# Kernel optimization log

Measured on AMD Instinct MI355X. Metric: run time of the kernel, lower is better.

Reference implementation:

```python
import jax, jax.numpy as jnp
import numpy as np
from jax import lax

H = 1024
W = 1024
WIN = 32
STR = 16
NH = (H - WIN) // STR + 1  # 63
N = NH * NH                # 3969 patches
DN3 = ('NCDHW', 'OIDHW', 'NCDHW')
DN2 = ('NCHW', 'OIHW', 'NCHW')


def setup_inputs() -> dict:
    key = jax.random.key(0)
    ks = jax.random.split(key, 13)
    r = lambda k, s, sc=0.05: jax.random.normal(k, s, dtype=jnp.float32) * sc
    return {
        'x1': jax.random.normal(ks[0], (1, 1, 1, H, W), jnp.float32),
        'x2': jax.random.normal(ks[1], (1, 1, 1, H, W), jnp.float32),
        'conv1_w': r(ks[2], (24, 1, 2, 8, 8)),      # Conv3d(1,24,(2,8,8)) [O,I,D,H,W]
        'conv1_b': r(ks[3], (24,)),
        'conv2_w': r(ks[4], (60, 24, 5, 5)),         # Conv2d(24,60,5)
        'conv2_b': r(ks[5], (60,)),
        'deconv2_w': r(ks[6], (60, 24, 5, 5)),       # ConvTranspose2d(60,24,5) [I,O,kH,kW]
        'deconv2_b': r(ks[7], (24,)),
        'deconv1_w': r(ks[8], (24, 1, 2, 8, 8)),     # ConvTranspose3d(24,1,(2,8,8)) [I,O,D,H,W]
        'deconv1_b': r(ks[9], (1,)),
        'lin_w': r(ks[10], (N, 2), 0.5),             # per-patch Linear(2,1) weights
        'lin_b': r(ks[11], (N,), 0.5),               # per-patch Linear(2,1) bias
        'linear1_w': r(ks[12], (1, 1), 0.5),         # Linear(1,1,bias=False)
    }


def _conv(x, w, b, dn):
    nd = w.ndim - 2
    y = lax.conv_general_dilated(x, w, (1,) * nd, 'VALID', dimension_numbers=dn)
    return y + b.reshape((1, -1) + (1,) * nd)


def _convT(x, w, b, dn):
    # stride-1, pad-0 transposed conv == full-pad conv with flipped, IO-swapped kernel
    nd = w.ndim - 2
    wf = jnp.flip(w, axis=tuple(range(2, w.ndim))).swapaxes(0, 1)  # [O,I,*k]
    pad = [(k - 1, k - 1) for k in w.shape[2:]]
    y = lax.conv_general_dilated(x, wf, (1,) * nd, pad, dimension_numbers=dn)
    return y + b.reshape((1, -1) + (1,) * nd)


def reference(x1, x2, conv1_w, conv1_b, conv2_w, conv2_b, deconv2_w, deconv2_b,
              deconv1_w, deconv1_b, lin_w, lin_b, linear1_w):
    x = jnp.concatenate([x1, x2], axis=2)[0, 0]  # [2,H,W]
    idx = (jnp.arange(NH) * STR)[:, None] + jnp.arange(WIN)[None, :]  # [NH,32]
    # unfold dims 3,4 with window 32 / stride 16 -> [2,NH,NW,32,32]
    patches = x[:, idx[:, None, :, None], idx[None, :, None, :]]
    outX = patches.reshape(2, N, WIN, WIN).transpose(1, 0, 2, 3)[:, None]  # [N,1,2,32,32]
    h = jax.nn.elu(_conv(outX, conv1_w, conv1_b, DN3))        # [N,24,1,25,25]
    h = jax.nn.relu(_conv(h[:, :, 0], conv2_w, conv2_b, DN2))  # [N,60,21,21]
    h = jax.nn.elu(_convT(h, deconv2_w, deconv2_b, DN2))       # [N,24,25,25]
    h = _convT(h[:, :, None], deconv1_w, deconv1_b, DN3)       # [N,1,2,32,32]
    # per-patch Linear(2,1) over depth channels, batched over all patches
    p = jnp.einsum('nchw,nc->nhw', h[:, 0], lin_w) + lin_b[:, None, None]  # [N,32,32]
    p = p.reshape(NH, NH, WIN, WIN)
    # col2im: overlap-add fold, block 32, stride 16 -> [H,W]
    recon = jnp.zeros((H, W), jnp.float32).at[idx[:, None, :, None], idx[None, :, None, :]].add(p)
    outX2 = recon * linear1_w[0, 0]  # Linear(1,1,bias=False) per pixel
    return x2 - outX2.reshape(x2.shape)
```

## Files before the change

### kernel.cpp

```cpp
#include <hip/hip_runtime.h>
#include <hip/hip_bf16.h>

static constexpr int H_ = 1024;
static constexpr int W_ = 1024;
static constexpr int STR_ = 16;
static constexpr int NH_ = 63;
static constexpr int NPATCH_ = NH_ * NH_;

typedef short bf16x8 __attribute__((ext_vector_type(8)));
typedef short short4v __attribute__((ext_vector_type(4)));
typedef float f32x4 __attribute__((ext_vector_type(4)));

static constexpr size_t FRAG_BYTES = 212992;
static constexpr size_t H1_SLAB    = 30768;
static constexpr size_t H2_SLAB    = 53248;
static constexpr size_t H1_BYTES   = (size_t)NPATCH_ * H1_SLAB;
static constexpr size_t H2_BYTES   = (size_t)NPATCH_ * H2_SLAB;
static constexpr size_t WS_NEED    = FRAG_BYTES + H1_BYTES + H2_BYTES;

__device__ __forceinline__ unsigned short f2bf(float x) {
    __hip_bfloat16 b = __float2bfloat16(x);
    return __builtin_bit_cast(unsigned short, b);
}

__device__ __forceinline__ f32x4 mfma_bf16(bf16x8 a, bf16x8 b, f32x4 c) {
    return __builtin_amdgcn_mfma_f32_16x16x32_bf16(a, b, c, 0, 0, 0);
}

__device__ __forceinline__ float elu_neg(float x) { return __expf(x) - 1.f; }

__global__ __launch_bounds__(256) void k_conv1(
    const float* __restrict__ x1, const float* __restrict__ x2,
    const float* __restrict__ c1b, const unsigned short* __restrict__ w1frag,
    unsigned short* __restrict__ h1)
{
    __shared__ alignas(16) char sbuf[10240];
    const int n = blockIdx.x, t = (int)threadIdx.x;
    const int pi = n / NH_, pj = n % NH_;
    const int Y0 = pi * STR_, X0 = pj * STR_;
    const int wv = t >> 6, lane = t & 63;
    const int ln15 = lane & 15, quad = lane >> 4;
    unsigned short* h1n = h1 + (size_t)n * (H1_SLAB / 2);

    bf16x8 w1b[8];
    #pragma unroll
    for (int g = 0; g < 8; ++g)
        w1b[g] = *(const bf16x8*)(w1frag + (g * 64 + lane) * 8);
    const f32x4 c1bq0 = *(const f32x4*)(c1b + quad * 4);
    f32x4 c1bq1 = (f32x4){0.f, 0.f, 0.f, 0.f};
    if (quad < 2) c1bq1 = *(const f32x4*)(c1b + 16 + quad * 4);

    if (t < 6) ((unsigned long long*)(h1n + 625 * 24))[t] = 0ull;

    for (int k = t; k < 2048; k += 256) {
        int d = k >> 10, r = k & 1023, y = r >> 5, x = r & 31;
        unsigned short bb = f2bf((d ? x2 : x1)[(Y0 + y) * W_ + (X0 + x)]);
        int row = (d * 32 + y) * 40;
        ((unsigned short*)(sbuf))[row + x] = bb;
        if (x > 0) ((unsigned short*)(sbuf + 5120))[row + x - 1] = bb;
    }
    __syncthreads();

    for (int tl = wv; tl < 40; tl += 4) {
        const int rawm = tl * 16 + ln15;
        int m = rawm > 624 ? 624 : rawm;
        int u = m / 25, v = m - u * 25;
        const char* cps = sbuf + ((v & 1) ? 5120 : 0);
        const int vb2 = (v & ~1) * 2;
        f32x4 acc0 = (f32x4){0.f, 0.f, 0.f, 0.f};
        f32x4 acc1 = (f32x4){0.f, 0.f, 0.f, 0.f};
        #pragma unroll
        for (int kc = 0; kc < 4; ++kc) {
            const int idx8 = kc * 4 + quad;
            const int dd = idx8 >> 3, pp = idx8 & 7;
            const unsigned int* ap = (const unsigned int*)(cps + (dd * 32 + u + pp) * 80 + vb2);
            union { unsigned int u4[4]; bf16x8 v8; } af;
            af.u4[0] = ap[0]; af.u4[1] = ap[1]; af.u4[2] = ap[2]; af.u4[3] = ap[3];
            acc0 = mfma_bf16(w1b[kc * 2 + 0], af.v8, acc0);
            acc1 = mfma_bf16(w1b[kc * 2 + 1], af.v8, acc1);
        }
        if (rawm < 625) {
            unsigned short* rowp = h1n + rawm * 24;
            short4v p0;
            #pragma unroll
            for (int r = 0; r < 4; ++r) {
                float hv = acc0[r] + c1bq0[r];
                hv = hv > 0.f ? hv : elu_neg(hv);
                p0[r] = (short)f2bf(hv);
            }
            *(short4v*)(rowp + quad * 4) = p0;
            if (quad < 2) {
                short4v p1;
                #pragma unroll
                for (int r = 0; r < 4; ++r) {
                    float hw = acc1[r] + c1bq1[r];
                    hw = hw > 0.f ? hw : elu_neg(hw);
                    p1[r] = (short)f2bf(hw);
                }
                *(short4v*)(rowp + 16 + quad * 4) = p1;
            }
        }
    }
}

__global__ __launch_bounds__(256) void k_conv2(
    const float* __restrict__ c2b, const unsigned short* __restrict__ w2frag,
    const unsigned short* __restrict__ h1, unsigned short* __restrict__ h2)
{
    __shared__ alignas(16) char sbuf[30048];
    const int n = blockIdx.x, t = (int)threadIdx.x;
    const int wv = t >> 6, lane = t & 63;
    const int ln15 = lane & 15, quad = lane >> 4;
    {
        const f32x4* src = (const f32x4*)(h1 + (size_t)n * (H1_SLAB / 2));
        f32x4* dst = (f32x4*)sbuf;
        for (int i = t; i < 1878; i += 256) dst[i] = src[i];
    }
    __syncthreads();

    const unsigned short* wb = w2frag + lane * 8;
    unsigned short* h2n = h2 + (size_t)n * (H2_SLAB / 2);

    for (int mt = wv; mt < 28; mt += 4) {
        int mm = mt * 16 + ln15; if (mm > 440) mm = 440;
        int y = mm / 21, x = mm - y * 21;
        const int abase = (y * 25 + x) * 48;
        f32x4 acc[4];
        #pragma unroll
        for (int nt = 0; nt < 4; ++nt) acc[nt] = (f32x4){0.f, 0.f, 0.f, 0.f};
        #pragma unroll
        for (int p = 0; p < 5; ++p) {
            #pragma unroll
            for (int q = 0; q < 5; ++q) {
                const int tap  = p * 5 + q;
                const int toff = (p * 25 + q) * 48;
                bf16x8 bfr[4];
                #pragma unroll
                for (int nt = 0; nt < 4; ++nt)
                    bfr[nt] = *(const bf16x8*)(wb + (tap * 4 + nt) * 512);
                bf16x8 a = *(const bf16x8*)(sbuf + abase + toff + quad * 16);
                #pragma unroll
                for (int nt = 0; nt < 4; ++nt)
                    acc[nt] = mfma_bf16(bfr[nt], a, acc[nt]);
            }
        }
        int rawpix = mt * 16 + ln15;
        if (rawpix < 441) {
            unsigned short* rowp = h2n + rawpix * 60;
            #pragma unroll
            for (int nt = 0; nt < 4; ++nt) {
                if (nt == 3 && quad == 3) continue;
                const f32x4 bq = *(const f32x4*)(c2b + nt * 16 + quad * 4);
                short4v pk;
                #pragma unroll
                for (int r = 0; r < 4; ++r)
                    pk[r] = (short)f2bf(fmaxf(acc[nt][r] + bq[r], 0.f));
                *(short4v*)(rowp + nt * 16 + quad * 4) = pk;
            }
        }
    }
}

__global__ __launch_bounds__(512) void k_deconv2(
    const float* __restrict__ d2b, const unsigned short* __restrict__ dw2frag,
    const unsigned short* __restrict__ h2, unsigned short* __restrict__ h3)
{
    __shared__ alignas(16) char sbuf[53056];
    const int n = blockIdx.x, t = (int)threadIdx.x;
    const int wv = t >> 6, lane = t & 63;
    const int ln15 = lane & 15, quad = lane >> 4;
    {
        const f32x4* src = (const f32x4*)(h2 + (size_t)n * (H2_SLAB / 2));
        f32x4* dst = (f32x4*)sbuf;
        for (int i = t; i < 3307; i += 512) dst[i] = src[i];
        if (t == 0)
            *(unsigned long long*)(sbuf + 52912) =
                *(const unsigned long long*)((const char*)src + 52912);
        if (t >= 64 && t < 81)
            ((unsigned long long*)(sbuf + 52920))[t - 64] = 0ull;
    }
    __syncthreads();

    const unsigned short* db = dw2frag + lane * 8;
    const f32x4 d2bq0 = *(const f32x4*)(d2b + quad * 4);
    f32x4 d2bq1 = (f32x4){0.f, 0.f, 0.f, 0.f};
    if (quad < 2) d2bq1 = *(const f32x4*)(d2b + 16 + quad * 4);
    unsigned short* h3n = h3 + (size_t)n * (H1_SLAB / 2);

    for (int mt = wv; mt < 40; mt += 8) {
        const int m = mt * 16 + ln15;
        const bool mv = (m < 625);
        const int mc = mv ? m : 0;
        const int ua = mc / 25, va = mc - ua * 25;
        const int aoff = (ua * 21 + va) * 120;
        f32x4 accN0 = (f32x4){0.f, 0.f, 0.f, 0.f};
        f32x4 accN1 = (f32x4){0.f, 0.f, 0.f, 0.f};
        #pragma unroll
        for (int dy = 0; dy < 5; ++dy) {
            #pragma unroll
            for (int dx = 0; dx < 5; ++dx) {
                const int tap = dy * 5 + dx;
                const int t2o = (dy * 21 + dx) * 120;
                bf16x8 bc0 = *(const bf16x8*)(db + tap * 2048);
                bf16x8 bc1 = *(const bf16x8*)(db + tap * 2048 + 512);
                bf16x8 bc2 = *(const bf16x8*)(db + tap * 2048 + 1024);
                bf16x8 bc3 = *(const bf16x8*)(db + tap * 2048 + 1536);
                int yv = ua - dy, xv = va - dx;
                bool ok = mv && ((unsigned)yv < 21u) && ((unsigned)xv < 21u);
                int ra = ok ? (aoff - t2o) : 52920;
                const char* ap = sbuf + ra + quad * 16;
                short4v lo0 = *(const short4v*)(ap);
                short4v hi0 = *(const short4v*)(ap + 8);
                bf16x8 a0 = __builtin_shufflevector(lo0, hi0, 0, 1, 2, 3, 4, 5, 6, 7);
                accN0 = mfma_bf16(bc0, a0, accN0);
                accN1 = mfma_bf16(bc1, a0, accN1);
                short4v lo1 = *(const short4v*)(ap + 64);
                short4v hi1 = *(const short4v*)(ap + 72);
                bf16x8 a1 = __builtin_shufflevector(lo1, hi1, 0, 1, 2, 3, 4, 5, 6, 7);
                accN0 = mfma_bf16(bc2, a1, accN0);
                accN1 = mfma_bf16(bc3, a1, accN1);
            }
        }
        if (m < 625) {
            unsigned short* rowp = h3n + m * 24;
            short4v p0;
            #pragma unroll
            for (int r = 0; r < 4; ++r) {
                float hv = accN0[r] + d2bq0[r];
                hv = hv > 0.f ? hv : elu_neg(hv);
                p0[r] = (short)f2bf(hv);
            }
            *(short4v*)(rowp + quad * 4) = p0;
            if (quad < 2) {
                short4v p1;
                #pragma unroll
                for (int r = 0; r < 4; ++r) {
                    float hw = accN1[r] + d2bq1[r];
                    hw = hw > 0.f ? hw : elu_neg(hw);
                    p1[r] = (short)f2bf(hw);
                }
                *(short4v*)(rowp + 16 + quad * 4) = p1;
            }
        }
    }
}

__global__ __launch_bounds__(256) void k_epilogue(
    const float* __restrict__ d1b, const float* __restrict__ lin_w,
    const float* __restrict__ lin_b, const float* __restrict__ dw1,
    const unsigned short* __restrict__ h3, float* __restrict__ recon)
{
    __shared__ alignas(16) char sbuf[38240];
    const int n = blockIdx.x, t = (int)threadIdx.x;
    const int pi = n / NH_, pj = n % NH_;
    const int Y0 = pi * STR_, X0 = pj * STR_;
    const int wv = t >> 6, lane = t & 63;
    const int ln15 = lane & 15, quad = lane >> 4;
    const float lw0 = lin_w[2 * n], lw1 = lin_w[2 * n + 1];
    {
        const f32x4* src = (const f32x4*)(h3 + (size_t)n * (H1_SLAB / 2));
        f32x4* dst = (f32x4*)sbuf;
        for (int i = t; i < 1878; i += 256) dst[i] = src[i];
    }
    unsigned short* swc = (unsigned short*)(sbuf + 30048);
    float* sp = (float*)(sbuf + 34144);
    for (int k = t; k < 2048; k += 256) {
        int r = k >> 5, c = k & 31;
        float v = 0.f;
        if (c < 24)
            v = lw0 * dw1[(c * 2 + 0) * 64 + r] + lw1 * dw1[(c * 2 + 1) * 64 + r];
        swc[r * 32 + c] = f2bf(v);
    }
    for (int k = t; k < 1024; k += 256) sp[k] = 0.f;
    __syncthreads();

    int qoff[4];
    #pragma unroll
    for (int r = 0; r < 4; ++r) {
        int qr = quad * 4 + r;
        qoff[r] = (qr >> 3) * 32 + (qr & 7);
    }
    for (int mt = wv; mt < 40; mt += 4) {
        int rawpix = mt * 16 + ln15;
        bool pok = (rawpix < 625);
        int pc = pok ? rawpix : 624;
        bf16x8 a = *(const bf16x8*)(sbuf + pc * 48 + quad * 16);
        int uvbase = (pc / 25) * 32 + (pc % 25);
        #pragma unroll
        for (int nt = 0; nt < 4; ++nt) {
            bf16x8 wbv = *(const bf16x8*)((char*)swc + (nt * 16 + ln15) * 64 + quad * 16);
            f32x4 a4 = (f32x4){0.f, 0.f, 0.f, 0.f};
            a4 = mfma_bf16(wbv, a, a4);
            if (pok) {
                #pragma unroll
                for (int r = 0; r < 4; ++r)
                    atomicAdd(&sp[uvbase + nt * 64 + qoff[r]], a4[r]);
            }
        }
    }
    __syncthreads();
    const float obias = d1b[0] * (lw0 + lw1) + lin_b[n];
    for (int k = t; k < 1024; k += 256) {
        int yy = k >> 5, xx = k & 31;
        atomicAdd(&recon[(Y0 + yy) * W_ + (X0 + xx)], sp[k] + obias);
    }
}

static constexpr int FGAP16 = 49200;
static constexpr int FCP0   = 49216;
static constexpr int FCP1   = 55360;
static constexpr int FSH2_0 = 49216;
static constexpr int FSH2SZ = 52920;
static constexpr int FSH2_1 = FSH2_0 + FSH2SZ;
static constexpr int FZROW  = 155056;
static constexpr int FH3SZ  = 30000;
static constexpr int FSWC0  = 60000;
static constexpr int FSWC1  = 64096;
static constexpr int FSPA   = 68192;
static constexpr int FLDS   = 155200;
static constexpr int FNGRP  = 32;
static constexpr int FNBLK  = NH_ * FNGRP;

__global__
__attribute__((amdgpu_flat_work_group_size(1024, 1024), amdgpu_waves_per_eu(4, 4)))
void fused_patch_kernel(
    const float* __restrict__ x1, const float* __restrict__ x2,
    const float* __restrict__ c1b, const float* __restrict__ c2b,
    const float* __restrict__ d2b, const float* __restrict__ d1b,
    const float* __restrict__ lin_w, const float* __restrict__ lin_b,
    const unsigned short* __restrict__ w1frag,
    const unsigned short* __restrict__ w2frag,
    const unsigned short* __restrict__ dw2frag,
    const float* __restrict__ dw1,
    float* __restrict__ recon)
{
    __shared__ alignas(16) char sbuf[FLDS];
    const int b   = blockIdx.x;
    const int pi  = b / FNGRP, g = b - pi * FNGRP;
    const int pj0 = 2 * g;
    const int npat = (pj0 + 1 < NH_) ? 2 : 1;
    const int n0  = pi * NH_ + pj0;
    const int n1  = (npat == 2) ? (n0 + 1) : n0;
    const int Y0  = pi * STR_, X0 = pj0 * STR_;
    const int t   = (int)threadIdx.x;
    const int wv  = t >> 6, lane = t & 63;
    const int ln15 = lane & 15, quad = lane >> 4;

    bf16x8 w1b[8];
    #pragma unroll
    for (int gg = 0; gg < 8; ++gg)
        w1b[gg] = *(const bf16x8*)(w1frag + (gg * 64 + lane) * 8);
    const float lw00 = lin_w[2 * n0], lw01 = lin_w[2 * n0 + 1];
    const float lw10 = lin_w[2 * n1], lw11 = lin_w[2 * n1 + 1];
    const float lbn0 = lin_b[n0], lbn1 = lin_b[n1];
    const float d1b0 = d1b[0];
    const f32x4 c1bq0 = *(const f32x4*)(c1b + quad * 4);
    f32x4 c1bq1 = (f32x4){0.f, 0.f, 0.f, 0.f};
    if (quad < 2) c1bq1 = *(const f32x4*)(c1b + 16 + quad * 4);
    const f32x4 d2bq0 = *(const f32x4*)(d2b + quad * 4);
    f32x4 d2bq1 = (f32x4){0.f, 0.f, 0.f, 0.f};
    if (quad < 2) d2bq1 = *(const f32x4*)(d2b + 16 + quad * 4);
    float dwp[4] = {0.f, 0.f, 0.f, 0.f};
    {
        int r0 = t >> 5, c0 = t & 31;
        if (c0 < 24) {
            dwp[0] = dw1[(c0 * 2 + 0) * 64 + r0];
            dwp[1] = dw1[(c0 * 2 + 1) * 64 + r0];
        }
        int k1 = t + 1024, r1 = k1 >> 5, c1 = k1 & 31;
        if (c1 < 24) {
            dwp[2] = dw1[(c1 * 2 + 0) * 64 + r1];
            dwp[3] = dw1[(c1 * 2 + 1) * 64 + r1];
        }
    }

    if (t < 4)       ((float*)(sbuf + FGAP16))[t] = 0.f;
    else if (t < 8)  ((float*)(sbuf + FSH2_1))[t - 4] = 0.f;
    else if (t < 42) ((float*)(sbuf + FZROW))[t - 8] = 0.f;
    #pragma unroll
    for (int it = 0; it < 3; ++it) {
        int k = t + it * 1024;
        int d = (k >= 1536) ? 1 : 0;
        int rem = k - d * 1536;
        int y = rem / 48, x = rem - y * 48;
        int xg = X0 + x; if (xg > W_ - 1) xg = W_ - 1;
        unsigned short bb = f2bf((d ? x2 : x1)[(Y0 + y) * W_ + xg]);
        int row = (d * 32 + y) * 48;
        ((unsigned short*)(sbuf + FCP0))[row + x] = bb;
        if (x > 0) ((unsigned short*)(sbuf + FCP1))[row + x - 1] = bb;
    }
    __syncthreads();

    for (int tl = wv; tl < 65; tl += 16) {
        const int rawm = tl * 16 + ln15;
        int m = rawm; if (m > 1024) m = 1024;
        int u = m / 41, v = m - u * 41;
        const char* cps = sbuf + ((v & 1) ? FCP1 : FCP0);
        const int vb2 = (v & ~1) * 2;
        f32x4 acc[2];
        acc[0] = (f32x4){0.f, 0.f, 0.f, 0.f};
        acc[1] = (f32x4){0.f, 0.f, 0.f, 0.f};
        #pragma unroll
        for (int kc = 0; kc < 4; ++kc) {
            const int idx8 = kc * 4 + quad;
            const int dd = idx8 >> 3, pp = idx8 & 7;
            const unsigned int* ap = (const unsigned int*)(cps + (dd * 32 + u + pp) * 96 + vb2);
            union { unsigned int u4[4]; bf16x8 v8; } af;
            af.u4[0] = ap[0]; af.u4[1] = ap[1]; af.u4[2] = ap[2]; af.u4[3] = ap[3];
            acc[0] = mfma_bf16(w1b[kc * 2 + 0], af.v8, acc[0]);
            acc[1] = mfma_bf16(w1b[kc * 2 + 1], af.v8, acc[1]);
        }
        if (rawm < 1025) {
            char* rowp = sbuf + rawm * 48;
            short4v p0;
            #pragma unroll
            for (int r = 0; r < 4; ++r) {
                float hv = acc[0][r] + c1bq0[r];
                hv = hv > 0.f ? hv : elu_neg(hv);
                p0[r] = (short)f2bf(hv);
            }
            *(short4v*)(rowp + quad * 8) = p0;
            if (quad < 2) {
                short4v p1;
                #pragma unroll
                for (int r = 0; r < 4; ++r) {
                    float hw = acc[1][r] + c1bq1[r];
                    hw = hw > 0.f ? hw : elu_neg(hw);
                    p1[r] = (short)f2bf(hw);
                }
                *(short4v*)(rowp + 32 + quad * 8) = p1;
            }
        }
    }
    __syncthreads();

    auto s2pass = [&](int t0, int t1) {
        const bool h1ok = (t1 < 56);
        int ab[2], loc[2], Pp[2];
        #pragma unroll
        for (int i = 0; i < 2; ++i) {
            int tt = i ? (h1ok ? t1 : t0) : t0;
            int P = (tt >= 28) ? 1 : 0;
            int lc = tt - P * 28;
            int mm = lc * 16 + ln15; if (mm > 440) mm = 440;
            int y = mm / 21, x = mm - y * 21;
            ab[i] = (y * 41 + P * 16 + x) * 48;
            loc[i] = lc; Pp[i] = P;
        }
        f32x4 acc2[2][4];
        #pragma unroll
        for (int i = 0; i < 2; ++i)
            #pragma unroll
            for (int nt = 0; nt < 4; ++nt)
                acc2[i][nt] = (f32x4){0.f, 0.f, 0.f, 0.f};
        const unsigned short* wb = w2frag + lane * 8;
        #pragma unroll
        for (int p = 0; p < 5; ++p) {
            #pragma unroll
            for (int q = 0; q < 5; ++q) {
                const int tap  = p * 5 + q;
                const int toff = (p * 41 + q) * 48;
                bf16x8 bfr[4];
                #pragma unroll
                for (int nt = 0; nt < 4; ++nt)
                    bfr[nt] = *(const bf16x8*)(wb + (tap * 4 + nt) * 512);
                {
                    bf16x8 a = *(const bf16x8*)(sbuf + ab[0] + toff + quad * 16);
                    #pragma unroll
                    for (int nt = 0; nt < 4; ++nt)
                        acc2[0][nt] = mfma_bf16(bfr[nt], a, acc2[0][nt]);
                }
                if (h1ok) {
                    bf16x8 a = *(const bf16x8*)(sbuf + ab[1] + toff + quad * 16);
                    #pragma unroll
                    for (int nt = 0; nt < 4; ++nt)
                        acc2[1][nt] = mfma_bf16(bfr[nt], a, acc2[1][nt]);
                }
            }
        }
        #pragma unroll
        for (int i = 0; i < 2; ++i) {
            if (i == 1 && !h1ok) continue;
            int rawpix = loc[i] * 16 + ln15;
            if (rawpix < 441) {
                char* rowp = sbuf + FSH2_0 + Pp[i] * FSH2SZ + rawpix * 120;
                #pragma unroll
                for (int nt = 0; nt < 4; ++nt) {
                    if (nt == 3 && quad == 3) continue;
                    const f32x4 bq = *(const f32x4*)(c2b + nt * 16 + quad * 4);
                    short4v pk;
                    #pragma unroll
                    for (int r = 0; r < 4; ++r)
                        pk[r] = (short)f2bf(fmaxf(acc2[i][nt][r] + bq[r], 0.f));
                    *(short4v*)(rowp + nt * 32 + quad * 8) = pk;
                }
            }
        }
    };
    s2pass(wv, wv + 16);
    s2pass(wv + 32, wv + 48);
    __syncthreads();

    f32x4 acc3[5][2];
    {
        #pragma unroll
        for (int i = 0; i < 5; ++i) {
            acc3[i][0] = (f32x4){0.f, 0.f, 0.f, 0.f};
            acc3[i][1] = (f32x4){0.f, 0.f, 0.f, 0.f};
        }
        int uarr[5], varr[5], aoff[5];
        bool mval[5];
        #pragma unroll
        for (int i = 0; i < 5; ++i) {
            int t5 = wv + 16 * i;
            int P = (t5 >= 40) ? 1 : 0;
            int lc = t5 - P * 40;
            int m = lc * 16 + ln15;
            mval[i] = (m < 625);
            int mc = mval[i] ? m : 0;
            uarr[i] = mc / 25; varr[i] = mc - uarr[i] * 25;
            aoff[i] = FSH2_0 + P * FSH2SZ + (uarr[i] * 21 + varr[i]) * 120;
        }
        const unsigned short* db = dw2frag + lane * 8;
        #pragma unroll
        for (int dy = 0; dy < 5; ++dy) {
            #pragma unroll
            for (int dx = 0; dx < 5; ++dx) {
                const int tap = dy * 5 + dx;
                const int t2o = (dy * 21 + dx) * 120;
                bf16x8 bc0 = *(const bf16x8*)(db + tap * 2048);
                bf16x8 bc1 = *(const bf16x8*)(db + tap * 2048 + 512);
                bf16x8 bc2 = *(const bf16x8*)(db + tap * 2048 + 1024);
                bf16x8 bc3 = *(const bf16x8*)(db + tap * 2048 + 1536);
                #pragma unroll
                for (int i = 0; i < 5; ++i) {
                    int yv = uarr[i] - dy, xv = varr[i] - dx;
                    bool ok = mval[i] && ((unsigned)yv < 21u) && ((unsigned)xv < 21u);
                    int ra = ok ? (aoff[i] - t2o) : FZROW;
                    const char* ap = sbuf + ra + quad * 16;
                    short4v lo0 = *(const short4v*)(ap);
                    short4v hi0 = *(const short4v*)(ap + 8);
                    bf16x8 a0 = __builtin_shufflevector(lo0, hi0, 0, 1, 2, 3, 4, 5, 6, 7);
                    acc3[i][0] = mfma_bf16(bc0, a0, acc3[i][0]);
                    acc3[i][1] = mfma_bf16(bc1, a0, acc3[i][1]);
                    short4v lo1 = *(const short4v*)(ap + 64);
                    short4v hi1 = *(const short4v*)(ap + 72);
                    bf16x8 a1 = __builtin_shufflevector(lo1, hi1, 0, 1, 2, 3, 4, 5, 6, 7);
                    acc3[i][0] = mfma_bf16(bc2, a1, acc3[i][0]);
                    acc3[i][1] = mfma_bf16(bc3, a1, acc3[i][1]);
                }
            }
        }
    }
    __syncthreads();

    float* sp = (float*)(sbuf + FSPA);
    {
        #pragma unroll
        for (int i = 0; i < 5; ++i) {
            int t5 = wv + 16 * i;
            int P = (t5 >= 40) ? 1 : 0;
            int lc = t5 - P * 40;
            int pix = lc * 16 + ln15;
            if (pix < 625) {
                char* rowp = sbuf + P * FH3SZ + pix * 48;
                short4v p0;
                #pragma unroll
                for (int r = 0; r < 4; ++r) {
                    float hv = acc3[i][0][r] + d2bq0[r];
                    hv = hv > 0.f ? hv : elu_neg(hv);
                    p0[r] = (short)f2bf(hv);
                }
                *(short4v*)(rowp + quad * 8) = p0;
                if (quad < 2) {
                    short4v p1;
                    #pragma unroll
                    for (int r = 0; r < 4; ++r) {
                        float hw = acc3[i][1][r] + d2bq1[r];
                        hw = hw > 0.f ? hw : elu_neg(hw);
                        p1[r] = (short)f2bf(hw);
                    }
                    *(short4v*)(rowp + 32 + quad * 8) = p1;
                }
            }
        }
    }
    {
        int r0 = t >> 5, c0 = t & 31;
        ((unsigned short*)(sbuf + FSWC0))[r0 * 32 + c0] = f2bf(lw00 * dwp[0] + lw01 * dwp[1]);
        ((unsigned short*)(sbuf + FSWC1))[r0 * 32 + c0] = f2bf(lw10 * dwp[0] + lw11 * dwp[1]);
        int k1 = t + 1024, r1 = k1 >> 5, c1 = k1 & 31;
        ((unsigned short*)(sbuf + FSWC0))[r1 * 32 + c1] = f2bf(lw00 * dwp[2] + lw01 * dwp[3]);
        ((unsigned short*)(sbuf + FSWC1))[r1 * 32 + c1] = f2bf(lw10 * dwp[2] + lw11 * dwp[3]);
    }
    sp[t] = 0.f; sp[t + 1024] = 0.f;
    __syncthreads();

    {
        int qoff[4];
        #pragma unroll
        for (int r = 0; r < 4; ++r) {
            int qr = quad * 4 + r;
            qoff[r] = (qr >> 3) * 32 + (qr & 7);
        }
        #pragma unroll
        for (int i = 0; i < 5; ++i) {
            int t5 = wv + 16 * i;
            int P = (t5 >= 40) ? 1 : 0;
            int lc = t5 - P * 40;
            int rawpix = lc * 16 + ln15;
            bool pok = (rawpix < 625);
            int pc = pok ? rawpix : 624;
            bf16x8 a = *(const bf16x8*)(sbuf + P * FH3SZ + pc * 48 + quad * 16);
            const char* swc = sbuf + (P ? FSWC1 : FSWC0);
            float* spP = sp + P * 1024;
            int uvbase = (pc / 25) * 32 + (pc % 25);
            #pragma unroll
            for (int nt = 0; nt < 4; ++nt) {
                bf16x8 wbv = *(const bf16x8*)(swc + (nt * 16 + ln15) * 64 + quad * 16);
                f32x4 acc4 = (f32x4){0.f, 0.f, 0.f, 0.f};
                acc4 = mfma_bf16(wbv, a, acc4);
                if (pok) {
                    #pragma unroll
                    for (int r = 0; r < 4; ++r)
                        atomicAdd(&spP[uvbase + nt * 64 + qoff[r]], acc4[r]);
                }
            }
        }
    }
    __syncthreads();

    {
        int yy = t >> 5, xx = t & 31;
        float ob0 = d1b0 * (lw00 + lw01) + lbn0;
        atomicAdd(&recon[(Y0 + yy) * W_ + X0 + xx], sp[t] + ob0);
        if (npat == 2) {
            float ob1 = d1b0 * (lw10 + lw11) + lbn1;
            atomicAdd(&recon[(Y0 + yy) * W_ + X0 + 16 + xx], sp[t + 1024] + ob1);
        }
    }
}

__global__ void prep_kernel(const float* __restrict__ c1w,
                            const float* __restrict__ c2w,
                            const float* __restrict__ d2w,
                            unsigned short* __restrict__ w1frag,
                            unsigned short* __restrict__ w2frag,
                            unsigned short* __restrict__ dw2frag)
{
    int i = blockIdx.x * blockDim.x + threadIdx.x;
    if (i < 51200) {
        int j = i & 7, lane = (i >> 3) & 63;
        int ln15 = lane & 15, quad = lane >> 4;
        if (i < 4096) {
            int g = i >> 9;
            int kc = g >> 1, nt = g & 1;
            int nn = nt * 16 + ln15, k = kc * 32 + quad * 8 + j;
            w1frag[i] = f2bf((nn < 24) ? c1w[nn * 128 + k] : 0.f);
        }
        {
            int nt = (i >> 9) & 3, tap = i >> 11;
            int o = nt * 16 + ln15, c = quad * 8 + j;
            float v = (o < 60 && c < 24) ? c2w[(o * 24 + c) * 25 + tap] : 0.f;
            w2frag[i] = f2bf(v);
        }
        {
            int nt = (i >> 9) & 1, kc = (i >> 10) & 1, tap = i >> 11;
            int k = kc * 32 + quad * 8 + j, c = nt * 16 + ln15;
            float v = (k < 60 && c < 24) ? d2w[(k * 24 + c) * 25 + tap] : 0.f;
            dw2frag[i] = f2bf(v);
        }
    }
}

__global__ void finalize_kernel(const float* __restrict__ x2,
                                const float* __restrict__ l1w,
                                float* __restrict__ out)
{
    int i = blockIdx.x * blockDim.x + threadIdx.x;
    if (i < H_ * W_) {
        float r = out[i];
        out[i] = x2[i] - r * l1w[0];
    }
}

extern "C" void kernel_launch(void* const* d_in, const int* in_sizes, int n_in,
                              void* d_out, int out_size, void* d_ws, size_t ws_size,
                              hipStream_t stream)
{
    const float* x1  = (const float*)d_in[0];
    const float* x2  = (const float*)d_in[1];
    const float* c1w = (const float*)d_in[2];
    const float* c1b = (const float*)d_in[3];
    const float* c2w = (const float*)d_in[4];
    const float* c2b = (const float*)d_in[5];
    const float* d2w = (const float*)d_in[6];
    const float* d2b = (const float*)d_in[7];
    const float* d1w = (const float*)d_in[8];
    const float* d1b = (const float*)d_in[9];
    const float* lw  = (const float*)d_in[10];
    const float* lb  = (const float*)d_in[11];
    const float* l1w = (const float*)d_in[12];

    float*          out     = (float*)d_out;
    unsigned short* w1frag  = (unsigned short*)d_ws;
    unsigned short* w2frag  = (unsigned short*)((char*)d_ws + 8192);
    unsigned short* dw2frag = (unsigned short*)((char*)d_ws + 110592);

    hipMemsetAsync(d_out, 0, (size_t)H_ * W_ * sizeof(float), stream);
    prep_kernel<<<100, 512, 0, stream>>>(c1w, c2w, d2w, w1frag, w2frag, dw2frag);

    if (ws_size >= WS_NEED) {
        unsigned short* h1 = (unsigned short*)((char*)d_ws + FRAG_BYTES);
        unsigned short* h2 = (unsigned short*)((char*)d_ws + FRAG_BYTES + H1_BYTES);
        unsigned short* h3 = h1;
        k_conv1<<<NPATCH_, 256, 0, stream>>>(x1, x2, c1b, w1frag, h1);
        k_conv2<<<NPATCH_, 256, 0, stream>>>(c2b, w2frag, h1, h2);
        k_deconv2<<<NPATCH_, 512, 0, stream>>>(d2b, dw2frag, h2, h3);
        k_epilogue<<<NPATCH_, 256, 0, stream>>>(d1b, lw, lb, d1w, h3, out);
    } else {
        fused_patch_kernel<<<FNBLK, 1024, 0, stream>>>(x1, x2, c1b, c2b, d2b, d1b,
                                                       lw, lb, w1frag, w2frag, dw2frag,
                                                       d1w, out);
    }
    finalize_kernel<<<(H_ * W_ + 255) / 256, 256, 0, stream>>>(x2, l1w, out);
}
```

Baseline: 1.340 ms.

## Fuse conv1+conv2 and deconv2+epilogue kernels, keep intermediates in LDS

Replaces the four per-patch kernels with two. The first computes conv1 into shared memory and feeds conv2 from there; the second computes deconv2 and immediately applies the folded deconv1/linear epilogue through a per-wave LDS scratch. This removes the global round-trips of the h1 and h3 intermediates and two launches. Patches are processed in chunks sized to the workspace, and launches now use 512 threads. The larger LDS footprint per block may reduce occupancy.

```diff
diff --git a/kernel.cpp b/kernel.cpp
--- a/kernel.cpp
+++ b/kernel.cpp
@@ -12,11 +12,7 @@
 typedef float f32x4 __attribute__((ext_vector_type(4)));
 
 static constexpr size_t FRAG_BYTES = 212992;
-static constexpr size_t H1_SLAB    = 30768;
 static constexpr size_t H2_SLAB    = 53248;
-static constexpr size_t H1_BYTES   = (size_t)NPATCH_ * H1_SLAB;
-static constexpr size_t H2_BYTES   = (size_t)NPATCH_ * H2_SLAB;
-static constexpr size_t WS_NEED    = FRAG_BYTES + H1_BYTES + H2_BYTES;
 
 __device__ __forceinline__ unsigned short f2bf(float x) {
     __hip_bfloat16 b = __float2bfloat16(x);
@@ -29,155 +25,165 @@
 
 __device__ __forceinline__ float elu_neg(float x) { return __expf(x) - 1.f; }
 
-__global__ __launch_bounds__(256) void k_conv1(
+__global__ __launch_bounds__(512) void k12(
     const float* __restrict__ x1, const float* __restrict__ x2,
-    const float* __restrict__ c1b, const unsigned short* __restrict__ w1frag,
-    unsigned short* __restrict__ h1)
+    const float* __restrict__ c1b, const float* __restrict__ c2b,
+    const unsigned short* __restrict__ w1frag,
+    const unsigned short* __restrict__ w2frag,
+    unsigned short* __restrict__ h2, int p0)
 {
-    __shared__ alignas(16) char sbuf[10240];
-    const int n = blockIdx.x, t = (int)threadIdx.x;
+    __shared__ alignas(16) char sbuf[40256];
+    const int n = p0 + (int)blockIdx.x;
+    const int t = (int)threadIdx.x;
     const int pi = n / NH_, pj = n % NH_;
     const int Y0 = pi * STR_, X0 = pj * STR_;
     const int wv = t >> 6, lane = t & 63;
     const int ln15 = lane & 15, quad = lane >> 4;
-    unsigned short* h1n = h1 + (size_t)n * (H1_SLAB / 2);
 
     bf16x8 w1b[8];
     #pragma unroll
     for (int g = 0; g < 8; ++g)
         w1b[g] = *(const bf16x8*)(w1frag + (g * 64 + lane) * 8);
-    const f32x4 c1bq0 = *(const f32x4*)(c1b + quad * 4);
-    f32x4 c1bq1 = (f32x4){0.f, 0.f, 0.f, 0.f};
-    if (quad < 2) c1bq1 = *(const f32x4*)(c1b + 16 + quad * 4);
-
-    if (t < 6) ((unsigned long long*)(h1n + 625 * 24))[t] = 0ull;
-
-    for (int k = t; k < 2048; k += 256) {
+
+    if (t < 4) ((float*)(sbuf + 30000))[t] = 0.f;
+    for (int k = t; k < 2048; k += 512) {
         int d = k >> 10, r = k & 1023, y = r >> 5, x = r & 31;
         unsigned short bb = f2bf((d ? x2 : x1)[(Y0 + y) * W_ + (X0 + x)]);
         int row = (d * 32 + y) * 40;
-        ((unsigned short*)(sbuf))[row + x] = bb;
-        if (x > 0) ((unsigned short*)(sbuf + 5120))[row + x - 1] = bb;
-    }
-    __syncthreads();
-
-    for (int tl = wv; tl < 40; tl += 4) {
-        const int rawm = tl * 16 + ln15;
-        int m = rawm > 624 ? 624 : rawm;
-        int u = m / 25, v = m - u * 25;
-        const char* cps = sbuf + ((v & 1) ? 5120 : 0);
-        const int vb2 = (v & ~1) * 2;
-        f32x4 acc0 = (f32x4){0.f, 0.f, 0.f, 0.f};
-        f32x4 acc1 = (f32x4){0.f, 0.f, 0.f, 0.f};
-        #pragma unroll
-        for (int kc = 0; kc < 4; ++kc) {
-            const int idx8 = kc * 4 + quad;
-            const int dd = idx8 >> 3, pp = idx8 & 7;
-            const unsigned int* ap = (const unsigned int*)(cps + (dd * 32 + u + pp) * 80 + vb2);
-            union { unsigned int u4[4]; bf16x8 v8; } af;
-            af.u4[0] = ap[0]; af.u4[1] = ap[1]; af.u4[2] = ap[2]; af.u4[3] = ap[3];
-            acc0 = mfma_bf16(w1b[kc * 2 + 0], af.v8, acc0);
-            acc1 = mfma_bf16(w1b[kc * 2 + 1], af.v8, acc1);
-        }
-        if (rawm < 625) {
-            unsigned short* rowp = h1n + rawm * 24;
-            short4v p0;
-            #pragma unroll
-            for (int r = 0; r < 4; ++r) {
-                float hv = acc0[r] + c1bq0[r];
-                hv = hv > 0.f ? hv : elu_neg(hv);
-                p0[r] = (short)f2bf(hv);
-            }
-            *(short4v*)(rowp + quad * 4) = p0;
-            if (quad < 2) {
-                short4v p1;
+        ((unsigned short*)(sbuf + 30016))[row + x] = bb;
+        if (x > 0) ((unsigned short*)(sbuf + 35136))[row + x - 1] = bb;
+    }
+    __syncthreads();
+
+    {
+        const f32x4 c1bq0 = *(const f32x4*)(c1b + quad * 4);
+        f32x4 c1bq1 = (f32x4){0.f, 0.f, 0.f, 0.f};
+        if (quad < 2) c1bq1 = *(const f32x4*)(c1b + 16 + quad * 4);
+        for (int tl = wv; tl < 40; tl += 8) {
+            const int rawm = tl * 16 + ln15;
+            int m = rawm > 624 ? 624 : rawm;
+            int u = m / 25, v = m - u * 25;
+            const char* cps = sbuf + ((v & 1) ? 35136 : 30016);
+            const int vb2 = (v & ~1) * 2;
+            f32x4 acc0 = (f32x4){0.f, 0.f, 0.f, 0.f};
+            f32x4 acc1 = (f32x4){0.f, 0.f, 0.f, 0.f};
+            #pragma unroll
+            for (int kc = 0; kc < 4; ++kc) {
+                const int idx8 = kc * 4 + quad;
+                const int dd = idx8 >> 3, pp = idx8 & 7;
+                const unsigned int* ap = (const unsigned int*)(cps + (dd * 32 + u + pp) * 80 + vb2);
+                union { unsigned int u4[4]; bf16x8 v8; } af;
+                af.u4[0] = ap[0]; af.u4[1] = ap[1]; af.u4[2] = ap[2]; af.u4[3] = ap[3];
+                acc0 = mfma_bf16(w1b[kc * 2 + 0], af.v8, acc0);
+                acc1 = mfma_bf16(w1b[kc * 2 + 1], af.v8, acc1);
+            }
+            if (rawm < 625) {
+                char* rowp = sbuf + rawm * 48;
+                short4v p0v;
                 #pragma unroll
                 for (int r = 0; r < 4; ++r) {
-                    float hw = acc1[r] + c1bq1[r];
-                    hw = hw > 0.f ? hw : elu_neg(hw);
-                    p1[r] = (short)f2bf(hw);
-                }
-                *(short4v*)(rowp + 16 + quad * 4) = p1;
+                    float hv = acc0[r] + c1bq0[r];
+                    hv = hv > 0.f ? hv : elu_neg(hv);
+                    p0v[r] = (short)f2bf(hv);
+                }
+                *(short4v*)(rowp + quad * 8) = p0v;
+                if (quad < 2) {
+                    short4v p1v;
+                    #pragma unroll
+                    for (int r = 0; r < 4; ++r) {
+                        float hw = acc1[r] + c1bq1[r];
+                        hw = hw > 0.f ? hw : elu_neg(hw);
+                        p1v[r] = (short)f2bf(hw);
+                    }
+                    *(short4v*)(rowp + 32 + quad * 8) = p1v;
+                }
+            }
+        }
+    }
+    __syncthreads();
+
+    {
+        const unsigned short* wb = w2frag + lane * 8;
+        unsigned short* h2g = h2 + (size_t)blockIdx.x * (H2_SLAB / 2);
+        for (int mt = wv; mt < 28; mt += 8) {
+            int mm = mt * 16 + ln15; if (mm > 440) mm = 440;
+            int y = mm / 21, x = mm - y * 21;
+            const int abase = (y * 25 + x) * 48;
+            f32x4 acc[4];
+            #pragma unroll
+            for (int nt = 0; nt < 4; ++nt) acc[nt] = (f32x4){0.f, 0.f, 0.f, 0.f};
+            #pragma unroll
+            for (int p = 0; p < 5; ++p) {
+                #pragma unroll
+                for (int q = 0; q < 5; ++q) {
+                    const int tap  = p * 5 + q;
+                    const int toff = (p * 25 + q) * 48;
+                    bf16x8 bfr[4];
+                    #pragma unroll
+                    for (int nt = 0; nt < 4; ++nt)
+                        bfr[nt] = *(const bf16x8*)(wb + (tap * 4 + nt) * 512);
+                    bf16x8 a = *(const bf16x8*)(sbuf + abase + toff + quad * 16);
+                    #pragma unroll
+                    for (int nt = 0; nt < 4; ++nt)
+                        acc[nt] = mfma_bf16(bfr[nt], a, acc[nt]);
+                }
+            }
+            int rawpix = mt * 16 + ln15;
+            if (rawpix < 441) {
+                unsigned short* rowp = h2g + rawpix * 60;
+                #pragma unroll
+                for (int nt = 0; nt < 4; ++nt) {
+                    if (nt == 3 && quad == 3) continue;
+                    const f32x4 bq = *(const f32x4*)(c2b + nt * 16 + quad * 4);
+                    short4v pk;
+                    #pragma unroll
+                    for (int r = 0; r < 4; ++r)
+                        pk[r] = (short)f2bf(fmaxf(acc[nt][r] + bq[r], 0.f));
+                    *(short4v*)(rowp + nt * 16 + quad * 4) = pk;
+                }
             }
         }
     }
 }
 
-__global__ __launch_bounds__(256) void k_conv2(
-    const float* __restrict__ c2b, const unsigned short* __restrict__ w2frag,
-    const unsigned short* __restrict__ h1, unsigned short* __restrict__ h2)
+__global__ __launch_bounds__(512) void k3e(
+    const float* __restrict__ d2b, const float* __restrict__ d1b,
+    const float* __restrict__ lin_w, const float* __restrict__ lin_b,
+    const float* __restrict__ dw1,
+    const unsigned short* __restrict__ dw2frag,
+    const unsigned short* __restrict__ h2, float* __restrict__ recon, int p0)
 {
-    __shared__ alignas(16) char sbuf[30048];
-    const int n = blockIdx.x, t = (int)threadIdx.x;
+    __shared__ alignas(16) char sbuf[70464];
+    const int n = p0 + (int)blockIdx.x;
+    const int t = (int)threadIdx.x;
+    const int pi = n / NH_, pj = n % NH_;
+    const int Y0 = pi * STR_, X0 = pj * STR_;
     const int wv = t >> 6, lane = t & 63;
     const int ln15 = lane & 15, quad = lane >> 4;
-    {
-        const f32x4* src = (const f32x4*)(h1 + (size_t)n * (H1_SLAB / 2));
-        f32x4* dst = (f32x4*)sbuf;
-        for (int i = t; i < 1878; i += 256) dst[i] = src[i];
-    }
-    __syncthreads();
-
-    const unsigned short* wb = w2frag + lane * 8;
-    unsigned short* h2n = h2 + (size_t)n * (H2_SLAB / 2);
-
-    for (int mt = wv; mt < 28; mt += 4) {
-        int mm = mt * 16 + ln15; if (mm > 440) mm = 440;
-        int y = mm / 21, x = mm - y * 21;
-        const int abase = (y * 25 + x) * 48;
-        f32x4 acc[4];
-        #pragma unroll
-        for (int nt = 0; nt < 4; ++nt) acc[nt] = (f32x4){0.f, 0.f, 0.f, 0.f};
-        #pragma unroll
-        for (int p = 0; p < 5; ++p) {
-            #pragma unroll
-            for (int q = 0; q < 5; ++q) {
-                const int tap  = p * 5 + q;
-                const int toff = (p * 25 + q) * 48;
-                bf16x8 bfr[4];
-                #pragma unroll
-                for (int nt = 0; nt < 4; ++nt)
-                    bfr[nt] = *(const bf16x8*)(wb + (tap * 4 + nt) * 512);
-                bf16x8 a = *(const bf16x8*)(sbuf + abase + toff + quad * 16);
-                #pragma unroll
-                for (int nt = 0; nt < 4; ++nt)
-                    acc[nt] = mfma_bf16(bfr[nt], a, acc[nt]);
-            }
-        }
-        int rawpix = mt * 16 + ln15;
-        if (rawpix < 441) {
-            unsigned short* rowp = h2n + rawpix * 60;
-            #pragma unroll
-            for (int nt = 0; nt < 4; ++nt) {
-                if (nt == 3 && quad == 3) continue;
-                const f32x4 bq = *(const f32x4*)(c2b + nt * 16 + quad * 4);
-                short4v pk;
-                #pragma unroll
-                for (int r = 0; r < 4; ++r)
-                    pk[r] = (short)f2bf(fmaxf(acc[nt][r] + bq[r], 0.f));
-                *(short4v*)(rowp + nt * 16 + quad * 4) = pk;
-            }
-        }
-    }
-}
-
-__global__ __launch_bounds__(512) void k_deconv2(
-    const float* __restrict__ d2b, const unsigned short* __restrict__ dw2frag,
-    const unsigned short* __restrict__ h2, unsigned short* __restrict__ h3)
-{
-    __shared__ alignas(16) char sbuf[53056];
-    const int n = blockIdx.x, t = (int)threadIdx.x;
-    const int wv = t >> 6, lane = t & 63;
-    const int ln15 = lane & 15, quad = lane >> 4;
-    {
-        const f32x4* src = (const f32x4*)(h2 + (size_t)n * (H2_SLAB / 2));
+    const float lw0 = lin_w[2 * n], lw1 = lin_w[2 * n + 1];
+
+    {
+        const f32x4* src = (const f32x4*)(h2 + (size_t)blockIdx.x * (H2_SLAB / 2));
         f32x4* dst = (f32x4*)sbuf;
         for (int i = t; i < 3307; i += 512) dst[i] = src[i];
-        if (t == 0)
+        if (t == 511)
             *(unsigned long long*)(sbuf + 52912) =
                 *(const unsigned long long*)((const char*)src + 52912);
-        if (t >= 64 && t < 81)
-            ((unsigned long long*)(sbuf + 52920))[t - 64] = 0ull;
+        if (t < 17) ((unsigned long long*)(sbuf + 52920))[t] = 0ull;
+    }
+    {
+        unsigned short* swc = (unsigned short*)(sbuf + 62272);
+        for (int k = t; k < 2048; k += 512) {
+            int r = k >> 5, c = k & 31;
+            float v = 0.f;
+            if (c < 24)
+                v = lw0 * dw1[(c * 2 + 0) * 64 + r] + lw1 * dw1[(c * 2 + 1) * 64 + r];
+            swc[r * 32 + c] = f2bf(v);
+        }
+    }
+    {
+        float* sp = (float*)(sbuf + 66368);
+        for (int k = t; k < 1024; k += 512) sp[k] = 0.f;
     }
     __syncthreads();
 
@@ -185,7 +191,18 @@
     const f32x4 d2bq0 = *(const f32x4*)(d2b + quad * 4);
     f32x4 d2bq1 = (f32x4){0.f, 0.f, 0.f, 0.f};
     if (quad < 2) d2bq1 = *(const f32x4*)(d2b + 16 + quad * 4);
-    unsigned short* h3n = h3 + (size_t)n * (H1_SLAB / 2);
+    bf16x8 wbv[4];
+    #pragma unroll
+    for (int nt = 0; nt < 4; ++nt)
+        wbv[nt] = *(const bf16x8*)(sbuf + 62272 + (nt * 16 + ln15) * 64 + quad * 16);
+    float* sp = (float*)(sbuf + 66368);
+    char* scr = sbuf + 53056 + wv * 1152;
+    int qoff[4];
+    #pragma unroll
+    for (int r = 0; r < 4; ++r) {
+        int qr = quad * 4 + r;
+        qoff[r] = (qr >> 3) * 32 + (qr & 7);
+    }
 
     for (int mt = wv; mt < 40; mt += 8) {
         const int m = mt * 16 + ln15;
@@ -221,77 +238,31 @@
                 accN1 = mfma_bf16(bc3, a1, accN1);
             }
         }
-        if (m < 625) {
-            unsigned short* rowp = h3n + m * 24;
-            short4v p0;
+        {
+            short4v p0v, p1v;
             #pragma unroll
             for (int r = 0; r < 4; ++r) {
                 float hv = accN0[r] + d2bq0[r];
                 hv = hv > 0.f ? hv : elu_neg(hv);
-                p0[r] = (short)f2bf(hv);
-            }
-            *(short4v*)(rowp + quad * 4) = p0;
-            if (quad < 2) {
-                short4v p1;
-                #pragma unroll
-                for (int r = 0; r < 4; ++r) {
-                    float hw = accN1[r] + d2bq1[r];
-                    hw = hw > 0.f ? hw : elu_neg(hw);
-                    p1[r] = (short)f2bf(hw);
-                }
-                *(short4v*)(rowp + 16 + quad * 4) = p1;
-            }
-        }
-    }
-}
-
-__global__ __launch_bounds__(256) void k_epilogue(
-    const float* __restrict__ d1b, const float* __restrict__ lin_w,
-    const float* __restrict__ lin_b, const float* __restrict__ dw1,
-    const unsigned short* __restrict__ h3, float* __restrict__ recon)
-{
-    __shared__ alignas(16) char sbuf[38240];
-    const int n = blockIdx.x, t = (int)threadIdx.x;
-    const int pi = n / NH_, pj = n % NH_;
-    const int Y0 = pi * STR_, X0 = pj * STR_;
-    const int wv = t >> 6, lane = t & 63;
-    const int ln15 = lane & 15, quad = lane >> 4;
-    const float lw0 = lin_w[2 * n], lw1 = lin_w[2 * n + 1];
-    {
-        const f32x4* src = (const f32x4*)(h3 + (size_t)n * (H1_SLAB / 2));
-        f32x4* dst = (f32x4*)sbuf;
-        for (int i = t; i < 1878; i += 256) dst[i] = src[i];
-    }
-    unsigned short* swc = (unsigned short*)(sbuf + 30048);
-    float* sp = (float*)(sbuf + 34144);
-    for (int k = t; k < 2048; k += 256) {
-        int r = k >> 5, c = k & 31;
-        float v = 0.f;
-        if (c < 24)
-            v = lw0 * dw1[(c * 2 + 0) * 64 + r] + lw1 * dw1[(c * 2 + 1) * 64 + r];
-        swc[r * 32 + c] = f2bf(v);
-    }
-    for (int k = t; k < 1024; k += 256) sp[k] = 0.f;
-    __syncthreads();
-
-    int qoff[4];
-    #pragma unroll
-    for (int r = 0; r < 4; ++r) {
-        int qr = quad * 4 + r;
-        qoff[r] = (qr >> 3) * 32 + (qr & 7);
-    }
-    for (int mt = wv; mt < 40; mt += 4) {
-        int rawpix = mt * 16 + ln15;
-        bool pok = (rawpix < 625);
-        int pc = pok ? rawpix : 624;
-        bf16x8 a = *(const bf16x8*)(sbuf + pc * 48 + quad * 16);
-        int uvbase = (pc / 25) * 32 + (pc % 25);
+                p0v[r] = (short)f2bf(hv);
+            }
+            #pragma unroll
+            for (int r = 0; r < 4; ++r) {
+                float hw = accN1[r] + d2bq1[r];
+                hw = hw > 0.f ? hw : elu_neg(hw);
+                p1v[r] = (short)f2bf(hw);
+            }
+            *(short4v*)(scr + ln15 * 72 + quad * 8) = p0v;
+            *(short4v*)(scr + ln15 * 72 + 32 + quad * 8) = p1v;
+        }
+        bf16x8 a = *(const bf16x8*)(scr + ln15 * 72 + quad * 16);
+        const int pc = mv ? m : 624;
+        const int uvbase = (pc / 25) * 32 + (pc % 25);
         #pragma unroll
         for (int nt = 0; nt < 4; ++nt) {
-            bf16x8 wbv = *(const bf16x8*)((char*)swc + (nt * 16 + ln15) * 64 + quad * 16);
             f32x4 a4 = (f32x4){0.f, 0.f, 0.f, 0.f};
-            a4 = mfma_bf16(wbv, a, a4);
-            if (pok) {
+            a4 = mfma_bf16(wbv[nt], a, a4);
+            if (mv) {
                 #pragma unroll
                 for (int r = 0; r < 4; ++r)
                     atomicAdd(&sp[uvbase + nt * 64 + qoff[r]], a4[r]);
@@ -299,8 +270,9 @@
         }
     }
     __syncthreads();
+
     const float obias = d1b[0] * (lw0 + lw1) + lin_b[n];
-    for (int k = t; k < 1024; k += 256) {
+    for (int k = t; k < 1024; k += 512) {
         int yy = k >> 5, xx = k & 31;
         atomicAdd(&recon[(Y0 + yy) * W_ + (X0 + xx)], sp[k] + obias);
     }
@@ -710,14 +682,17 @@
     hipMemsetAsync(d_out, 0, (size_t)H_ * W_ * sizeof(float), stream);
     prep_kernel<<<100, 512, 0, stream>>>(c1w, c2w, d2w, w1frag, w2frag, dw2frag);
 
-    if (ws_size >= WS_NEED) {
-        unsigned short* h1 = (unsigned short*)((char*)d_ws + FRAG_BYTES);
-        unsigned short* h2 = (unsigned short*)((char*)d_ws + FRAG_BYTES + H1_BYTES);
-        unsigned short* h3 = h1;
-        k_conv1<<<NPATCH_, 256, 0, stream>>>(x1, x2, c1b, w1frag, h1);
-        k_conv2<<<NPATCH_, 256, 0, stream>>>(c2b, w2frag, h1, h2);
-        k_deconv2<<<NPATCH_, 512, 0, stream>>>(d2b, dw2frag, h2, h3);
-        k_epilogue<<<NPATCH_, 256, 0, stream>>>(d1b, lw, lb, d1w, h3, out);
+    size_t avail = (ws_size > FRAG_BYTES) ? (ws_size - FRAG_BYTES) : 0;
+    size_t ppg_s = avail / H2_SLAB;
+    int ppg = (ppg_s > (size_t)NPATCH_) ? NPATCH_ : (int)ppg_s;
+
+    if (ppg >= 100) {
+        unsigned short* h2 = (unsigned short*)((char*)d_ws + FRAG_BYTES);
+        for (int p0 = 0; p0 < NPATCH_; p0 += ppg) {
+            int cnt = NPATCH_ - p0; if (cnt > ppg) cnt = ppg;
+            k12<<<cnt, 512, 0, stream>>>(x1, x2, c1b, c2b, w1frag, w2frag, h2, p0);
+            k3e<<<cnt, 512, 0, stream>>>(d2b, d1b, lw, lb, d1w, dw2frag, h2, out, p0);
+        }
     } else {
         fused_patch_kernel<<<FNBLK, 1024, 0, stream>>>(x1, x2, c1b, c2b, d2b, d1b,
                                                        lw, lb, w1frag, w2frag, dw2frag,
```

Result: slower. 3.692 ms (+175.4%).
